# Kernel tuning notes

Measured on AMD Instinct MI355X. Metric: run time of the kernel, lower is better.

The kernel has to match this reference:

```python
import jax, jax.numpy as jnp
import numpy as np

N_NODES = 100000
N_EDGES = 1600000
IN_DIM = 128
OUT_DIM = 32
HEADS = 4
EDGE_DIM = 32
N_ETYPES = 8
NEG_SLOPE = 0.2


def setup_inputs() -> dict:
    key = jax.random.key(0)
    ks = jax.random.split(key, 12)
    return {
        "h": jax.random.normal(ks[0], (N_NODES, IN_DIM), jnp.float32),
        "row": jax.random.randint(ks[1], (N_EDGES,), 0, N_NODES),
        "col": jax.random.randint(ks[2], (N_EDGES,), 0, N_NODES),
        "etype": jax.random.randint(ks[3], (N_EDGES,), 0, N_ETYPES),
        "edge_emb": jax.random.normal(ks[4], (N_ETYPES, EDGE_DIM), jnp.float32),
        "W": jax.random.normal(ks[5], (IN_DIM, OUT_DIM * HEADS), jnp.float32) * 0.1,
        "W_r_w": jax.random.normal(ks[6], (N_ETYPES, EDGE_DIM, EDGE_DIM * HEADS), jnp.float32) * 0.1,
        "a_l": jax.random.normal(ks[7], (1, HEADS, OUT_DIM), jnp.float32) * 0.1,
        "a_r": jax.random.normal(ks[8], (1, HEADS, OUT_DIM), jnp.float32) * 0.1,
        "a_e": jax.random.normal(ks[9], (1, HEADS, EDGE_DIM), jnp.float32) * 0.1,
        "res_w": jax.random.normal(ks[10], (IN_DIM, OUT_DIM * HEADS), jnp.float32) * 0.1,
        "res_b": jax.random.normal(ks[11], (OUT_DIM * HEADS,), jnp.float32) * 0.1,
    }


def reference(h, row, col, etype, edge_emb, W, W_r_w, a_l, a_r, a_e, res_w, res_b):
    N = h.shape[0]
    # node projection: (N, heads, out_dim)
    emb = (h @ W).reshape(N, HEADS, OUT_DIM)
    # TypedLinear on per-etype embeddings: compute once per etype, gather per edge
    typed = jnp.einsum('te,teo->to', edge_emb, W_r_w).reshape(N_ETYPES, HEADS, EDGE_DIM)
    e_emb = typed[etype]                                   # (E, heads, edge_dim)
    # attention logits
    h_l = jnp.sum(a_l * emb, axis=-1)                      # (N, heads)
    h_r = jnp.sum(a_r * emb, axis=-1)                      # (N, heads)
    h_e = jnp.sum(a_e * e_emb, axis=-1)                    # (E, heads)
    logits = jax.nn.leaky_relu(h_l[row] + h_r[col] + h_e, NEG_SLOPE)
    # edge softmax over incoming edges of each destination node (col)
    m = jax.ops.segment_max(logits, col, num_segments=N)   # (N, heads)
    ex = jnp.exp(logits - m[col])
    den = jax.ops.segment_sum(ex, col, num_segments=N)
    alpha = ex / den[col]                                  # (E, heads)
    # weighted scatter-sum aggregation: u_mul_e + sum onto dst
    msg = emb[row] * alpha[:, :, None]                     # (E, heads, out_dim)
    agg = jax.ops.segment_sum(msg, col, num_segments=N)    # (N, heads, out_dim)
    # original permutes emb to (N, out_dim, heads) before flattening
    h_out = jnp.transpose(agg, (0, 2, 1)).reshape(N, OUT_DIM * HEADS)
    h_out = h_out + h @ res_w + res_b                      # residual
    return jax.nn.elu(h_out)
```

## Files before the change

kernel.cpp:

```cpp
#include <hip/hip_runtime.h>

#define NNODES 100000
#define NEDGES 1600000
#define INDIM 128
#define OUTD 32
#define HEADS 4
#define EDIM 32
#define NET 8
#define NEG 0.2f
#define CAP 64
#define SB 1600
#define GB2 782
#define CSTRIDE 16

typedef unsigned short u16;
typedef unsigned int u32;
typedef __attribute__((ext_vector_type(8))) short bf16x8;
typedef __attribute__((ext_vector_type(8))) unsigned short ushort8;
typedef __attribute__((ext_vector_type(4))) float f32x4;

__device__ __forceinline__ float bf2f(u16 u){ return __uint_as_float(((u32)u) << 16); }
__device__ __forceinline__ u16 f2bf(float f){
  u32 x = __float_as_uint(f);
  return (u16)((x + 0x7fffu + ((x >> 16) & 1u)) >> 16);
}

__global__ void k_prep(const float* __restrict__ edge_emb, const float* __restrict__ Wr,
                       const float* __restrict__ a_e, const float* __restrict__ W,
                       const float* __restrict__ res_w,
                       float* __restrict__ he_t, u16* __restrict__ Wt,
                       int* __restrict__ cnt){
  const int b = blockIdx.x, tid = threadIdx.x;
  int4 z4 = make_int4(0, 0, 0, 0);
  for (int i = b * 256 + tid; i < NNODES * CSTRIDE / 4; i += gridDim.x * 256)
    ((int4*)cnt)[i] = z4;

  if (b == 0){
    __shared__ float sc[NET * 128];
    for (int idx = tid; idx < NET * 128; idx += 256){
      int t = idx >> 7, o = idx & 127;
      float s = 0.f;
      #pragma unroll
      for (int e = 0; e < EDIM; ++e)
        s += edge_emb[t * EDIM + e] * Wr[t * EDIM * 128 + e * 128 + o];
      sc[idx] = s * a_e[o];
    }
    __syncthreads();
    if (tid < NET * HEADS){
      int t = tid >> 2, h = tid & 3;
      float s = 0.f;
      #pragma unroll
      for (int d = 0; d < EDIM; ++d) s += sc[t * 128 + h * EDIM + d];
      he_t[tid] = s;
    }
  } else {
    int idx = (b - 1) * 256 + tid;
    int n = idx >> 7, k = idx & 127;
    float v = (n < 128) ? W[k * 128 + n] : res_w[k * 128 + (n - 128)];
    Wt[idx] = f2bf(v);
  }
}

__global__ __launch_bounds__(256) void k_main(
    const float* __restrict__ hmat, const u16* __restrict__ Wt,
    const float* __restrict__ res_b, const float* __restrict__ a_l,
    const float* __restrict__ a_r, u16* __restrict__ emb, float* __restrict__ outres,
    float* __restrict__ h_l, float* __restrict__ h_r,
    const int* __restrict__ row, const int* __restrict__ col,
    const int* __restrict__ et, int* __restrict__ cnt, int* __restrict__ rtp){
  __shared__ u16 Wl[128 * 136];
  const int tid = threadIdx.x;

  if (blockIdx.x < SB){
    for (int e = blockIdx.x * 256 + tid; e < NEDGES; e += SB * 256){
      int c = col[e];
      int pos = atomicAdd(&cnt[c * CSTRIDE], 1);
      if (pos < CAP) rtp[c * CAP + pos] = row[e] | (et[e] << 17);
    }
    return;
  }

  const int gb = blockIdx.x - SB;
  const int wid = tid >> 6, lane = tid & 63;
  const int m0 = gb * 128 + wid * 32;
  const int mcol = lane & 15, quad = lane >> 4;

  bf16x8 A[2][4];
  #pragma unroll
  for (int mt = 0; mt < 2; ++mt){
    int r = m0 + mt * 16 + mcol;
    int rc = r < NNODES ? r : NNODES - 1;
    const float* hrow = &hmat[rc * 128 + quad * 8];
    #pragma unroll
    for (int ks = 0; ks < 4; ++ks){
      float4 a0 = *(const float4*)&hrow[ks * 32];
      float4 a1 = *(const float4*)&hrow[ks * 32 + 4];
      A[mt][ks][0] = (short)f2bf(a0.x); A[mt][ks][1] = (short)f2bf(a0.y);
      A[mt][ks][2] = (short)f2bf(a0.z); A[mt][ks][3] = (short)f2bf(a0.w);
      A[mt][ks][4] = (short)f2bf(a1.x); A[mt][ks][5] = (short)f2bf(a1.y);
      A[mt][ks][6] = (short)f2bf(a1.z); A[mt][ks][7] = (short)f2bf(a1.w);
    }
  }

  float pl[2][4] = {}, pr[2][4] = {};
  #pragma unroll
  for (int phase = 0; phase < 2; ++phase){
    if (phase) __syncthreads();
    #pragma unroll
    for (int j = 0; j < 8; ++j){
      int cid = tid + j * 256;
      int rowL = cid >> 4, k8 = cid & 15;
      *(uint4*)&Wl[rowL * 136 + k8 * 8] =
          *(const uint4*)&Wt[(phase * 128 + rowL) * 128 + k8 * 8];
    }
    __syncthreads();

    #pragma unroll
    for (int ntl = 0; ntl < 8; ++ntl){
      bf16x8 B[4];
      const u16* bp = &Wl[(ntl * 16 + mcol) * 136 + quad * 8];
      #pragma unroll
      for (int ks = 0; ks < 4; ++ks) B[ks] = *(const bf16x8*)&bp[ks * 32];

      f32x4 acc[2] = {{0.f,0.f,0.f,0.f},{0.f,0.f,0.f,0.f}};
      #pragma unroll
      for (int ks = 0; ks < 4; ++ks){
        acc[0] = __builtin_amdgcn_mfma_f32_16x16x32_bf16(A[0][ks], B[ks], acc[0], 0, 0, 0);
        acc[1] = __builtin_amdgcn_mfma_f32_16x16x32_bf16(A[1][ks], B[ks], acc[1], 0, 0, 0);
      }

      const int c = ntl * 16 + mcol;
      if (phase == 0){
        float alc = a_l[c], arc = a_r[c];
        #pragma unroll
        for (int mt = 0; mt < 2; ++mt){
          #pragma unroll
          for (int reg = 0; reg < 4; ++reg){
            int rw = m0 + mt * 16 + quad * 4 + reg;
            if (rw < NNODES) emb[rw * 128 + c] = f2bf(acc[mt][reg]);
            pl[mt][reg] += alc * acc[mt][reg];
            pr[mt][reg] += arc * acc[mt][reg];
          }
        }
        if (ntl & 1){
          int h = ntl >> 1;
          #pragma unroll
          for (int mt = 0; mt < 2; ++mt){
            #pragma unroll
            for (int reg = 0; reg < 4; ++reg){
              float s0 = pl[mt][reg], s1 = pr[mt][reg];
              #pragma unroll
              for (int off = 1; off < 16; off <<= 1){
                s0 += __shfl_xor(s0, off, 64);
                s1 += __shfl_xor(s1, off, 64);
              }
              int rw = m0 + mt * 16 + quad * 4 + reg;
              if (mcol == 0 && rw < NNODES){
                h_l[rw * 4 + h] = s0;
                h_r[rw * 4 + h] = s1;
              }
              pl[mt][reg] = 0.f; pr[mt][reg] = 0.f;
            }
          }
        }
      } else {
        float rb = res_b[c];
        #pragma unroll
        for (int mt = 0; mt < 2; ++mt){
          #pragma unroll
          for (int reg = 0; reg < 4; ++reg){
            int rw = m0 + mt * 16 + quad * 4 + reg;
            if (rw < NNODES) outres[rw * 128 + c] = acc[mt][reg] + rb;
          }
        }
      }
    }
  }
}

__global__ __launch_bounds__(256) void k_nodeagg(const int* __restrict__ cnt,
    const int* __restrict__ rtp, const float* __restrict__ h_l,
    const float* __restrict__ h_r, const float* __restrict__ he_t_g,
    const u16* __restrict__ emb, float* __restrict__ out){
  __shared__ float wl[4][CAP][4];
  __shared__ int   rl[4][CAP];

  const int wid = threadIdx.x >> 6;
  const int n = blockIdx.x * 4 + wid;
  const int lane = threadIdx.x & 63;
  int deg = cnt[n * CSTRIDE]; if (deg > CAP) deg = CAP;
  const int base = n * CAP;

  {
    bool v = lane < deg;
    int rt = rtp[base + (v ? lane : 0)];
    int r = rt & 0x1FFFF, t = (rt >> 17) & 7;
    float4 hl = *(const float4*)&h_l[r * 4];
    float4 hr = *(const float4*)&h_r[n * 4];
    float4 he = *(const float4*)&he_t_g[t * 4];
    float x0 = hl.x + hr.x + he.x; x0 = x0 > 0.f ? x0 : NEG * x0;
    float x1 = hl.y + hr.y + he.y; x1 = x1 > 0.f ? x1 : NEG * x1;
    float x2 = hl.z + hr.z + he.z; x2 = x2 > 0.f ? x2 : NEG * x2;
    float x3 = hl.w + hr.w + he.w; x3 = x3 > 0.f ? x3 : NEG * x3;
    float4 w4 = make_float4(__expf(x0), __expf(x1), __expf(x2), __expf(x3));
    *(float4*)&wl[wid][lane][0] = w4;
    rl[wid][lane] = r;
  }
  __syncthreads();

  const int q = lane >> 4;
  const int L = lane & 15;
  const int h = L >> 2;

  float acc[8] = {0.f,0.f,0.f,0.f,0.f,0.f,0.f,0.f};
  float ds = 0.f;
  for (int i = 0; i < deg; i += 8){
    int i0 = i + q, i1 = i + 4 + q;
    bool v0 = i0 < deg, v1 = i1 < deg;
    int ii0 = v0 ? i0 : 0, ii1 = v1 ? i1 : 0;
    int r0 = rl[wid][ii0];
    int r1 = rl[wid][ii1];
    float w0 = v0 ? wl[wid][ii0][h] : 0.f;
    float w1 = v1 ? wl[wid][ii1][h] : 0.f;
    ushort8 u0 = *(const ushort8*)&emb[r0 * 128 + L * 8];
    ushort8 u1 = *(const ushort8*)&emb[r1 * 128 + L * 8];
    #pragma unroll
    for (int k = 0; k < 8; ++k) acc[k] += w0 * bf2f((u16)u0[k]);
    ds += w0;
    #pragma unroll
    for (int k = 0; k < 8; ++k) acc[k] += w1 * bf2f((u16)u1[k]);
    ds += w1;
  }

  #pragma unroll
  for (int k = 0; k < 8; ++k){
    acc[k] += __shfl_xor(acc[k], 16, 64);
    acc[k] += __shfl_xor(acc[k], 32, 64);
  }
  ds += __shfl_xor(ds, 16, 64);
  ds += __shfl_xor(ds, 32, 64);

  if (q == 0){
    float inv = (deg > 0) ? 1.f / ds : 0.f;
    int ob = n * 128 + (L & 3) * 32 + (L >> 2);
    #pragma unroll
    for (int k = 0; k < 8; ++k){
      int o = ob + k * 4;
      float v = acc[k] * inv + out[o];
      out[o] = v > 0.f ? v : (__expf(v) - 1.f);
    }
  }
}

extern "C" void kernel_launch(void* const* d_in, const int* in_sizes, int n_in,
                              void* d_out, int out_size, void* d_ws, size_t ws_size,
                              hipStream_t stream){
  const float* hmat     = (const float*)d_in[0];
  const int*   row      = (const int*)d_in[1];
  const int*   col      = (const int*)d_in[2];
  const int*   et       = (const int*)d_in[3];
  const float* edge_emb = (const float*)d_in[4];
  const float* W        = (const float*)d_in[5];
  const float* Wr       = (const float*)d_in[6];
  const float* a_l      = (const float*)d_in[7];
  const float* a_r      = (const float*)d_in[8];
  const float* a_e      = (const float*)d_in[9];
  const float* res_w    = (const float*)d_in[10];
  const float* res_b    = (const float*)d_in[11];
  float* out = (float*)d_out;

  char* ws = (char*)d_ws;
  float* he_t   = (float*)(ws);
  u16*   Wt     = (u16*)  (ws + 256);
  float* h_l    = (float*)(ws + 65792);
  float* h_r    = (float*)(ws + 1665792);
  int*   cnt    = (int*)  (ws + 3265792);
  int*   rtp    = (int*)  (ws + 9665792);
  u16*   emb    = (u16*)  (ws + 35265792);

  hipLaunchKernelGGL(k_prep, dim3(129), dim3(256), 0, stream,
                     edge_emb, Wr, a_e, W, res_w, he_t, Wt, cnt);
  hipLaunchKernelGGL(k_main, dim3(SB + GB2), dim3(256), 0, stream,
                     hmat, Wt, res_b, a_l, a_r, emb, out, h_l, h_r,
                     row, col, et, cnt, rtp);
  hipLaunchKernelGGL(k_nodeagg, dim3(NNODES / 4), dim3(256), 0, stream,
                     cnt, rtp, h_l, h_r, he_t, emb, out);
}
```

Before: 364.5 us.

## Vectorize edge bucketing with 8 edges per thread and read weights from global

The edge-bucketing blocks now process 8 consecutive edges per thread using int4 loads, issuing eight independent atomics per thread, and use 782 blocks instead of 1600 grid-strided blocks. The GEMM blocks drop the shared-memory staging of the bf16 weight matrix and its syncthreads, loading B fragments straight from global memory (L2-cached). This frees LDS and removes barriers, which should raise occupancy, but it relies on cache hits for the repeated weight reads, and the strided row-wise B loads may be less efficient than LDS reads.

```diff
diff --git a/kernel.cpp b/kernel.cpp
--- a/kernel.cpp
+++ b/kernel.cpp
@@ -9,7 +9,7 @@
 #define NET 8
 #define NEG 0.2f
 #define CAP 64
-#define SB 1600
+#define SB2 782
 #define GB2 782
 #define CSTRIDE 16
 
@@ -68,19 +68,39 @@
     float* __restrict__ h_l, float* __restrict__ h_r,
     const int* __restrict__ row, const int* __restrict__ col,
     const int* __restrict__ et, int* __restrict__ cnt, int* __restrict__ rtp){
-  __shared__ u16 Wl[128 * 136];
   const int tid = threadIdx.x;
 
-  if (blockIdx.x < SB){
-    for (int e = blockIdx.x * 256 + tid; e < NEDGES; e += SB * 256){
-      int c = col[e];
-      int pos = atomicAdd(&cnt[c * CSTRIDE], 1);
-      if (pos < CAP) rtp[c * CAP + pos] = row[e] | (et[e] << 17);
+  if (blockIdx.x < SB2){
+    int s = blockIdx.x * 256 + tid;
+    if (s < NEDGES / 8){
+      const int e0 = s * 8;
+      int4 c0 = *(const int4*)&col[e0];
+      int4 c1 = *(const int4*)&col[e0 + 4];
+      int4 r0 = *(const int4*)&row[e0];
+      int4 r1 = *(const int4*)&row[e0 + 4];
+      int4 t0 = *(const int4*)&et[e0];
+      int4 t1 = *(const int4*)&et[e0 + 4];
+      int p0 = atomicAdd(&cnt[c0.x * CSTRIDE], 1);
+      int p1 = atomicAdd(&cnt[c0.y * CSTRIDE], 1);
+      int p2 = atomicAdd(&cnt[c0.z * CSTRIDE], 1);
+      int p3 = atomicAdd(&cnt[c0.w * CSTRIDE], 1);
+      int p4 = atomicAdd(&cnt[c1.x * CSTRIDE], 1);
+      int p5 = atomicAdd(&cnt[c1.y * CSTRIDE], 1);
+      int p6 = atomicAdd(&cnt[c1.z * CSTRIDE], 1);
+      int p7 = atomicAdd(&cnt[c1.w * CSTRIDE], 1);
+      if (p0 < CAP) rtp[c0.x * CAP + p0] = r0.x | (t0.x << 17);
+      if (p1 < CAP) rtp[c0.y * CAP + p1] = r0.y | (t0.y << 17);
+      if (p2 < CAP) rtp[c0.z * CAP + p2] = r0.z | (t0.z << 17);
+      if (p3 < CAP) rtp[c0.w * CAP + p3] = r0.w | (t0.w << 17);
+      if (p4 < CAP) rtp[c1.x * CAP + p4] = r1.x | (t1.x << 17);
+      if (p5 < CAP) rtp[c1.y * CAP + p5] = r1.y | (t1.y << 17);
+      if (p6 < CAP) rtp[c1.z * CAP + p6] = r1.z | (t1.z << 17);
+      if (p7 < CAP) rtp[c1.w * CAP + p7] = r1.w | (t1.w << 17);
     }
     return;
   }
 
-  const int gb = blockIdx.x - SB;
+  const int gb = blockIdx.x - SB2;
   const int wid = tid >> 6, lane = tid & 63;
   const int m0 = gb * 128 + wid * 32;
   const int mcol = lane & 15, quad = lane >> 4;
@@ -105,20 +125,10 @@
   float pl[2][4] = {}, pr[2][4] = {};
   #pragma unroll
   for (int phase = 0; phase < 2; ++phase){
-    if (phase) __syncthreads();
-    #pragma unroll
-    for (int j = 0; j < 8; ++j){
-      int cid = tid + j * 256;
-      int rowL = cid >> 4, k8 = cid & 15;
-      *(uint4*)&Wl[rowL * 136 + k8 * 8] =
-          *(const uint4*)&Wt[(phase * 128 + rowL) * 128 + k8 * 8];
-    }
-    __syncthreads();
-
     #pragma unroll
     for (int ntl = 0; ntl < 8; ++ntl){
       bf16x8 B[4];
-      const u16* bp = &Wl[(ntl * 16 + mcol) * 136 + quad * 8];
+      const u16* bp = &Wt[(phase * 128 + ntl * 16 + mcol) * 128 + quad * 8];
       #pragma unroll
       for (int ks = 0; ks < 4; ++ks) B[ks] = *(const bf16x8*)&bp[ks * 32];
 
@@ -280,7 +290,7 @@
 
   hipLaunchKernelGGL(k_prep, dim3(129), dim3(256), 0, stream,
                      edge_emb, Wr, a_e, W, res_w, he_t, Wt, cnt);
-  hipLaunchKernelGGL(k_main, dim3(SB + GB2), dim3(256), 0, stream,
+  hipLaunchKernelGGL(k_main, dim3(SB2 + GB2), dim3(256), 0, stream,
                      hmat, Wt, res_b, a_l, a_r, emb, out, h_l, h_r,
                      row, col, et, cnt, rtp);
   hipLaunchKernelGGL(k_nodeagg, dim3(NNODES / 4), dim3(256), 0, stream,
```

Measured after the change: 360.6 us. No clear change (-1.1%).
